# Kernel tuning notes

Hardware: AMD Instinct MI355X
Metric: run time of the kernel (lower is better)

Reference implementation:

```python
import jax, jax.numpy as jnp
import numpy as np

MASK_VALUE = -1e6


def setup_inputs() -> dict:
    key = jax.random.key(0)
    ks = jax.random.split(key, 8)
    B, Lq, Lk, D, H = 4, 512, 512, 128, 128
    return {
        "queries": jax.random.normal(ks[0], (B, Lq, D), dtype=jnp.float32),
        "keys": jax.random.normal(ks[1], (B, Lk, D), dtype=jnp.float32),
        "values": jax.random.normal(ks[2], (B, Lk, D), dtype=jnp.float32),
        "valid_seq_len": jax.random.randint(ks[3], (B,), 1, Lk + 1),
        "Wq": jax.random.normal(ks[4], (D, H), dtype=jnp.float32) * 0.05,
        "Wk": jax.random.normal(ks[5], (D, H), dtype=jnp.float32) * 0.05,
        "wv": jax.random.normal(ks[6], (H,), dtype=jnp.float32) * 0.05,
        "Wo": jax.random.normal(ks[7], (D, H), dtype=jnp.float32) * 0.05,
    }


def reference(queries, keys, values, valid_seq_len, Wq, Wk, wv, Wo):
    # q: (B,Lq,H), k: (B,Lk,H)
    q = jnp.einsum("bqd,dh->bqh", queries, Wq)
    k = jnp.einsum("bkd,dh->bkh", keys, Wk)
    # additive features: (B,Lq,Lk,H) -> scalar scores via wv
    feat = jnp.tanh(q[:, :, None, :] + k[:, None, :, :])
    scores = jnp.einsum("bqkh,h->bqk", feat, wv)
    # mask invalid key positions per batch (softmax over last dim)
    Lk = keys.shape[1]
    mask = jnp.arange(Lk)[None, None, :] < valid_seq_len[:, None, None]
    scores = jnp.where(mask, scores, MASK_VALUE)
    attn = jax.nn.softmax(scores, axis=-1)  # (B,Lq,Lk)
    out = jnp.einsum("bqk,bkd->bqd", attn, values)
    return jnp.einsum("bqd,dh->bqh", out, Wo)
```

## Files before the change

### kernel.cpp

```cpp
#include <hip/hip_runtime.h>
#include <hip/hip_bf16.h>

#define B_   4
#define LQ   512
#define LK   512
#define D_   128
#define H_   128
#define LKP  576
#define QSS  2
#define QSF  4

#define TWO_LOG2E 2.885390081777927f
#define LOG2E     1.442695040888963f

__device__ __forceinline__ float fexp2(float x) {
#if __has_builtin(__builtin_amdgcn_exp2f)
  return __builtin_amdgcn_exp2f(x);
#else
  return exp2f(x);
#endif
}
__device__ __forceinline__ float frcp(float x) {
#if __has_builtin(__builtin_amdgcn_rcpf)
  return __builtin_amdgcn_rcpf(x);
#else
  return __fdividef(1.0f, x);
#endif
}

__device__ __forceinline__ void sig4(float eqa, float eqb, float w, float2 ek,
                                     float& aA0, float& aA1, float& aB0, float& aB1) {
  float dA0 = fmaf(eqa, ek.x, 1.f);
  float dA1 = fmaf(eqa, ek.y, 1.f);
  float RA  = frcp(dA0 * dA1);
  aA0 = fmaf(w * dA1, RA, aA0);
  aA1 = fmaf(w * dA0, RA, aA1);
  float dB0 = fmaf(eqb, ek.x, 1.f);
  float dB1 = fmaf(eqb, ek.y, 1.f);
  float RB  = frcp(dB0 * dB1);
  aB0 = fmaf(w * dB1, RB, aB0);
  aB1 = fmaf(w * dB0, RB, aB1);
}

__global__ __launch_bounds__(256) void proj_kernel(
    const float* __restrict__ queries, const float* __restrict__ keys,
    const float* __restrict__ Wq, const float* __restrict__ Wk,
    float* __restrict__ Eq, float* __restrict__ EkT) {
  __shared__ float s_x[8][D_];
  int r0 = blockIdx.x * 8;
  bool qside = r0 < B_ * LQ;
  const float* X = qside ? queries : keys;
  const float* W = qside ? Wq : Wk;
  int rb = qside ? r0 : r0 - B_ * LQ;
  int tid = threadIdx.x;
  for (int i = tid; i < 8 * D_; i += 256)
    s_x[i >> 7][i & 127] = X[(size_t)(rb + (i >> 7)) * D_ + (i & 127)];
  __syncthreads();
  int h = tid & 127, rh = tid >> 7;
  const float4* x0 = (const float4*)s_x[rh * 4 + 0];
  const float4* x1 = (const float4*)s_x[rh * 4 + 1];
  const float4* x2 = (const float4*)s_x[rh * 4 + 2];
  const float4* x3 = (const float4*)s_x[rh * 4 + 3];
  float a0 = 0.f, a1 = 0.f, a2 = 0.f, a3 = 0.f;
  #pragma unroll 8
  for (int d4 = 0; d4 < D_ / 4; ++d4) {
    float4 xa = x0[d4], xb = x1[d4], xc = x2[d4], xd = x3[d4];
    const float* Wd = W + 4 * d4 * H_ + h;
    float w0 = Wd[0], w1 = Wd[H_], w2 = Wd[2 * H_], w3 = Wd[3 * H_];
    a0 = fmaf(xa.x, w0, fmaf(xa.y, w1, fmaf(xa.z, w2, fmaf(xa.w, w3, a0))));
    a1 = fmaf(xb.x, w0, fmaf(xb.y, w1, fmaf(xb.z, w2, fmaf(xb.w, w3, a1))));
    a2 = fmaf(xc.x, w0, fmaf(xc.y, w1, fmaf(xc.z, w2, fmaf(xc.w, w3, a2))));
    a3 = fmaf(xd.x, w0, fmaf(xd.y, w1, fmaf(xd.z, w2, fmaf(xd.w, w3, a3))));
  }
  if (qside) {
    Eq[(size_t)(rb + rh * 4 + 0) * H_ + h] = fexp2(a0 * TWO_LOG2E);
    Eq[(size_t)(rb + rh * 4 + 1) * H_ + h] = fexp2(a1 * TWO_LOG2E);
    Eq[(size_t)(rb + rh * 4 + 2) * H_ + h] = fexp2(a2 * TWO_LOG2E);
    Eq[(size_t)(rb + rh * 4 + 3) * H_ + h] = fexp2(a3 * TWO_LOG2E);
  } else {
    int b = rb >> 9, kk = (rb & 511) + rh * 4;
    float* dst = EkT + ((size_t)b * H_ + h) * LKP + kk;
    dst[0] = fexp2(a0 * TWO_LOG2E);
    dst[1] = fexp2(a1 * TWO_LOG2E);
    dst[2] = fexp2(a2 * TWO_LOG2E);
    dst[3] = fexp2(a3 * TWO_LOG2E);
  }
}

__global__ __launch_bounds__(256) void score_kernel(
    const float* __restrict__ Eq, const float* __restrict__ EkT,
    const int* __restrict__ vlen_arr, const float* __restrict__ wv,
    float* __restrict__ sc_g) {
  int id = blockIdx.x;
  int b = id & 3, q0 = (id >> 2) * QSS;
  int tid = threadIdx.x;

  __shared__ float s_eq[QSS][H_];
  __shared__ float s_wv[H_];

  s_eq[tid >> 7][tid & 127] = Eq[(size_t)(b * LQ + q0 + (tid >> 7)) * H_ + (tid & 127)];
  if (tid < H_) s_wv[tid] = wv[tid];
  __syncthreads();
  int vlen = vlen_arr[b];

  const float4* wv4p = (const float4*)s_wv;
  float sum_wv = 0.f;
  #pragma unroll
  for (int j = 0; j < H_ / 4; ++j) {
    float4 t4 = wv4p[j];
    sum_wv += t4.x + t4.y + t4.z + t4.w;
  }

  int k0 = tid * 2;
  if (k0 < vlen) {
    const float2* ek2 = (const float2*)(EkT + (size_t)b * H_ * LKP);
    const float4* eqa4 = (const float4*)s_eq[0];
    const float4* eqb4 = (const float4*)s_eq[1];
    float aA0 = 0.f, aA1 = 0.f, aB0 = 0.f, aB1 = 0.f;
    #pragma unroll 2
    for (int h4 = 0; h4 < H_ / 4; ++h4) {
      float2 e0 = ek2[(size_t)(4 * h4 + 0) * (LKP / 2) + tid];
      float2 e1 = ek2[(size_t)(4 * h4 + 1) * (LKP / 2) + tid];
      float2 e2 = ek2[(size_t)(4 * h4 + 2) * (LKP / 2) + tid];
      float2 e3 = ek2[(size_t)(4 * h4 + 3) * (LKP / 2) + tid];
      float4 w4 = wv4p[h4];
      float4 qa = eqa4[h4];
      float4 qb = eqb4[h4];
      sig4(qa.x, qb.x, w4.x, e0, aA0, aA1, aB0, aB1);
      sig4(qa.y, qb.y, w4.y, e1, aA0, aA1, aB0, aB1);
      sig4(qa.z, qb.z, w4.z, e2, aA0, aA1, aB0, aB1);
      sig4(qa.w, qb.w, w4.w, e3, aA0, aA1, aB0, aB1);
    }
    float2 rA = { fmaf(-2.f, aA0, sum_wv), fmaf(-2.f, aA1, sum_wv) };
    float2 rB = { fmaf(-2.f, aB0, sum_wv), fmaf(-2.f, aB1, sum_wv) };
    ((float2*)(sc_g + (size_t)(b * LQ + q0 + 0) * LK))[tid] = rA;
    ((float2*)(sc_g + (size_t)(b * LQ + q0 + 1) * LK))[tid] = rB;
  }
}

__global__ __launch_bounds__(256) void finish_kernel(
    const float* __restrict__ sc_g, const float* __restrict__ values,
    const int* __restrict__ vlen_arr, const float* __restrict__ Wo,
    float* __restrict__ out) {
  int id = blockIdx.x;
  int b = id & 3, q0 = (id >> 2) * QSF;
  int tid = threadIdx.x, wave = tid >> 6, lane = tid & 63;
  int vlen = vlen_arr[b];

  __shared__ float s_w[QSF][LK];
  __shared__ float s_po[QSF][QSF][D_];
  __shared__ float s_pr[QSF][D_];

  {
    const float* srow = sc_g + (size_t)(b * LQ + q0 + wave) * LK;
    float vals[LK / 64];
    float m = -3.0e38f;
    #pragma unroll
    for (int j = 0; j < LK / 64; ++j) {
      int k = lane + j * 64;
      float v = (k < vlen) ? srow[k] : -1.0e30f;
      vals[j] = v;
      m = fmaxf(m, v);
    }
    #pragma unroll
    for (int off = 32; off; off >>= 1) m = fmaxf(m, __shfl_xor(m, off));
    float sum = 0.f;
    #pragma unroll
    for (int j = 0; j < LK / 64; ++j) {
      float e = fexp2((vals[j] - m) * LOG2E);
      vals[j] = e;
      sum += e;
    }
    #pragma unroll
    for (int off = 32; off; off >>= 1) sum += __shfl_xor(sum, off);
    float inv = frcp(sum);
    #pragma unroll
    for (int j = 0; j < LK / 64; ++j) s_w[wave][lane + j * 64] = vals[j] * inv;
  }
  __syncthreads();

  {
    int kbeg = wave * 128;
    int kend = min((vlen + 3) & ~3, kbeg + 128);
    const float2* vrow = (const float2*)(values + (size_t)b * LK * D_);
    float2 a0 = {0.f, 0.f}, a1 = {0.f, 0.f}, a2 = {0.f, 0.f}, a3 = {0.f, 0.f};
    #pragma unroll 2
    for (int kk = kbeg; kk < kend; kk += 4) {
      float2 v0 = vrow[(size_t)(kk + 0) * 64 + lane];
      float2 v1 = vrow[(size_t)(kk + 1) * 64 + lane];
      float2 v2 = vrow[(size_t)(kk + 2) * 64 + lane];
      float2 v3 = vrow[(size_t)(kk + 3) * 64 + lane];
      float4 w0 = *(const float4*)&s_w[0][kk];
      float4 w1 = *(const float4*)&s_w[1][kk];
      float4 w2 = *(const float4*)&s_w[2][kk];
      float4 w3 = *(const float4*)&s_w[3][kk];
      a0.x += w0.x * v0.x + w0.y * v1.x + w0.z * v2.x + w0.w * v3.x;
      a0.y += w0.x * v0.y + w0.y * v1.y + w0.z * v2.y + w0.w * v3.y;
      a1.x += w1.x * v0.x + w1.y * v1.x + w1.z * v2.x + w1.w * v3.x;
      a1.y += w1.x * v0.y + w1.y * v1.y + w1.z * v2.y + w1.w * v3.y;
      a2.x += w2.x * v0.x + w2.y * v1.x + w2.z * v2.x + w2.w * v3.x;
      a2.y += w2.x * v0.y + w2.y * v1.y + w2.z * v2.y + w2.w * v3.y;
      a3.x += w3.x * v0.x + w3.y * v1.x + w3.z * v2.x + w3.w * v3.x;
      a3.y += w3.x * v0.y + w3.y * v1.y + w3.z * v2.y + w3.w * v3.y;
    }
    s_po[wave][0][2 * lane] = a0.x; s_po[wave][0][2 * lane + 1] = a0.y;
    s_po[wave][1][2 * lane] = a1.x; s_po[wave][1][2 * lane + 1] = a1.y;
    s_po[wave][2][2 * lane] = a2.x; s_po[wave][2][2 * lane + 1] = a2.y;
    s_po[wave][3][2 * lane] = a3.x; s_po[wave][3][2 * lane + 1] = a3.y;
  }
  __syncthreads();

  #pragma unroll
  for (int i = tid; i < QSF * D_; i += 256) {
    int r = i >> 7, d = i & 127;
    s_pr[r][d] = s_po[0][r][d] + s_po[1][r][d] + s_po[2][r][d] + s_po[3][r][d];
  }
  __syncthreads();

  {
    int h = tid & 127, r = tid >> 7;
    float accA = 0.f, accB = 0.f;
    #pragma unroll 8
    for (int d = 0; d < D_; ++d) {
      float w = Wo[d * H_ + h];
      accA = fmaf(s_pr[r][d], w, accA);
      accB = fmaf(s_pr[r + 2][d], w, accB);
    }
    out[(size_t)(b * LQ + q0 + r) * H_ + h] = accA;
    out[(size_t)(b * LQ + q0 + r + 2) * H_ + h] = accB;
  }
}

extern "C" void kernel_launch(void* const* d_in, const int* in_sizes, int n_in,
                              void* d_out, int out_size, void* d_ws, size_t ws_size,
                              hipStream_t stream) {
  const float* queries = (const float*)d_in[0];
  const float* keys    = (const float*)d_in[1];
  const float* values  = (const float*)d_in[2];
  const int*   vlen    = (const int*)d_in[3];
  const float* Wq      = (const float*)d_in[4];
  const float* Wk      = (const float*)d_in[5];
  const float* wv      = (const float*)d_in[6];
  const float* Wo      = (const float*)d_in[7];
  float* out = (float*)d_out;

  float* Eq   = (float*)d_ws;
  float* EkT  = Eq + (size_t)B_ * LQ * H_;
  float* sc_g = EkT + (size_t)B_ * H_ * LKP;

  proj_kernel<<<dim3(B_ * (LQ + LK) / 8), 256, 0, stream>>>(queries, keys, Wq, Wk, Eq, EkT);
  score_kernel<<<dim3(B_ * (LQ / QSS)), 256, 0, stream>>>(Eq, EkT, vlen, wv, sc_g);
  finish_kernel<<<dim3(B_ * (LQ / QSF)), 256, 0, stream>>>(sc_g, values, vlen, Wo, out);
}
```

Measured before the change: 117.2 us.

## Widen score and PV register tiles to float4 per thread

The score kernel now handles four query rows per block and four keys per thread, with float4 loads of EkT. Each loaded key vector is reused across two query rows per thread, and the number of score blocks is halved. The finish kernel's PV loop switches to float4 value loads, splitting the keys across half-waves, and combines the halves with a cross-lane shuffle. The aim is fewer load instructions and more register reuse, at the cost of higher register pressure and fewer blocks in the score grid.

```diff
diff --git a/kernel.cpp b/kernel.cpp
--- a/kernel.cpp
+++ b/kernel.cpp
@@ -7,7 +7,7 @@
 #define D_   128
 #define H_   128
 #define LKP  576
-#define QSS  2
+#define QSS  4
 #define QSF  4
 
 #define TWO_LOG2E 2.885390081777927f
@@ -28,18 +28,17 @@
 #endif
 }
 
-__device__ __forceinline__ void sig4(float eqa, float eqb, float w, float2 ek,
-                                     float& aA0, float& aA1, float& aB0, float& aB1) {
-  float dA0 = fmaf(eqa, ek.x, 1.f);
-  float dA1 = fmaf(eqa, ek.y, 1.f);
-  float RA  = frcp(dA0 * dA1);
-  aA0 = fmaf(w * dA1, RA, aA0);
-  aA1 = fmaf(w * dA0, RA, aA1);
-  float dB0 = fmaf(eqb, ek.x, 1.f);
-  float dB1 = fmaf(eqb, ek.y, 1.f);
-  float RB  = frcp(dB0 * dB1);
-  aB0 = fmaf(w * dB1, RB, aB0);
-  aB1 = fmaf(w * dB0, RB, aB1);
+__device__ __forceinline__ void sig4k(float eq, float w, float4 ek, float4& acc) {
+  float d0 = fmaf(eq, ek.x, 1.f);
+  float d1 = fmaf(eq, ek.y, 1.f);
+  float d2 = fmaf(eq, ek.z, 1.f);
+  float d3 = fmaf(eq, ek.w, 1.f);
+  float R01 = frcp(d0 * d1);
+  float R23 = frcp(d2 * d3);
+  acc.x = fmaf(w * d1, R01, acc.x);
+  acc.y = fmaf(w * d0, R01, acc.y);
+  acc.z = fmaf(w * d3, R23, acc.z);
+  acc.w = fmaf(w * d2, R23, acc.w);
 }
 
 __global__ __launch_bounds__(256) void proj_kernel(
@@ -98,7 +97,8 @@
   __shared__ float s_eq[QSS][H_];
   __shared__ float s_wv[H_];
 
-  s_eq[tid >> 7][tid & 127] = Eq[(size_t)(b * LQ + q0 + (tid >> 7)) * H_ + (tid & 127)];
+  for (int i = tid; i < QSS * H_; i += 256)
+    s_eq[i >> 7][i & 127] = Eq[(size_t)(b * LQ + q0 + (i >> 7)) * H_ + (i & 127)];
   if (tid < H_) s_wv[tid] = wv[tid];
   __syncthreads();
   int vlen = vlen_arr[b];
@@ -111,30 +111,34 @@
     sum_wv += t4.x + t4.y + t4.z + t4.w;
   }
 
-  int k0 = tid * 2;
+  int kq = tid & 127, rp = tid >> 7;
+  int k0 = kq * 4;
   if (k0 < vlen) {
-    const float2* ek2 = (const float2*)(EkT + (size_t)b * H_ * LKP);
-    const float4* eqa4 = (const float4*)s_eq[0];
-    const float4* eqb4 = (const float4*)s_eq[1];
-    float aA0 = 0.f, aA1 = 0.f, aB0 = 0.f, aB1 = 0.f;
+    const float4* ekp = (const float4*)(EkT + (size_t)b * H_ * LKP);
+    const float4* qa4 = (const float4*)s_eq[2 * rp + 0];
+    const float4* qb4 = (const float4*)s_eq[2 * rp + 1];
+    float4 accA = {0.f, 0.f, 0.f, 0.f};
+    float4 accB = {0.f, 0.f, 0.f, 0.f};
     #pragma unroll 2
     for (int h4 = 0; h4 < H_ / 4; ++h4) {
-      float2 e0 = ek2[(size_t)(4 * h4 + 0) * (LKP / 2) + tid];
-      float2 e1 = ek2[(size_t)(4 * h4 + 1) * (LKP / 2) + tid];
-      float2 e2 = ek2[(size_t)(4 * h4 + 2) * (LKP / 2) + tid];
-      float2 e3 = ek2[(size_t)(4 * h4 + 3) * (LKP / 2) + tid];
+      float4 e0 = ekp[(size_t)(4 * h4 + 0) * (LKP / 4) + kq];
+      float4 e1 = ekp[(size_t)(4 * h4 + 1) * (LKP / 4) + kq];
+      float4 e2 = ekp[(size_t)(4 * h4 + 2) * (LKP / 4) + kq];
+      float4 e3 = ekp[(size_t)(4 * h4 + 3) * (LKP / 4) + kq];
       float4 w4 = wv4p[h4];
-      float4 qa = eqa4[h4];
-      float4 qb = eqb4[h4];
-      sig4(qa.x, qb.x, w4.x, e0, aA0, aA1, aB0, aB1);
-      sig4(qa.y, qb.y, w4.y, e1, aA0, aA1, aB0, aB1);
-      sig4(qa.z, qb.z, w4.z, e2, aA0, aA1, aB0, aB1);
-      sig4(qa.w, qb.w, w4.w, e3, aA0, aA1, aB0, aB1);
-    }
-    float2 rA = { fmaf(-2.f, aA0, sum_wv), fmaf(-2.f, aA1, sum_wv) };
-    float2 rB = { fmaf(-2.f, aB0, sum_wv), fmaf(-2.f, aB1, sum_wv) };
-    ((float2*)(sc_g + (size_t)(b * LQ + q0 + 0) * LK))[tid] = rA;
-    ((float2*)(sc_g + (size_t)(b * LQ + q0 + 1) * LK))[tid] = rB;
+      float4 qa = qa4[h4];
+      float4 qb = qb4[h4];
+      sig4k(qa.x, w4.x, e0, accA);  sig4k(qb.x, w4.x, e0, accB);
+      sig4k(qa.y, w4.y, e1, accA);  sig4k(qb.y, w4.y, e1, accB);
+      sig4k(qa.z, w4.z, e2, accA);  sig4k(qb.z, w4.z, e2, accB);
+      sig4k(qa.w, w4.w, e3, accA);  sig4k(qb.w, w4.w, e3, accB);
+    }
+    float4 rA = { fmaf(-2.f, accA.x, sum_wv), fmaf(-2.f, accA.y, sum_wv),
+                  fmaf(-2.f, accA.z, sum_wv), fmaf(-2.f, accA.w, sum_wv) };
+    float4 rB = { fmaf(-2.f, accB.x, sum_wv), fmaf(-2.f, accB.y, sum_wv),
+                  fmaf(-2.f, accB.z, sum_wv), fmaf(-2.f, accB.w, sum_wv) };
+    ((float4*)(sc_g + (size_t)(b * LQ + q0 + 2 * rp + 0) * LK))[kq] = rA;
+    ((float4*)(sc_g + (size_t)(b * LQ + q0 + 2 * rp + 1) * LK))[kq] = rB;
   }
 }
 
@@ -182,31 +186,51 @@
   {
     int kbeg = wave * 128;
     int kend = min((vlen + 3) & ~3, kbeg + 128);
-    const float2* vrow = (const float2*)(values + (size_t)b * LK * D_);
-    float2 a0 = {0.f, 0.f}, a1 = {0.f, 0.f}, a2 = {0.f, 0.f}, a3 = {0.f, 0.f};
-    #pragma unroll 2
+    const float4* v4 = (const float4*)(values + (size_t)b * LK * D_);
+    int dq = lane & 31, kpar = lane >> 5;
+    float4 a0 = {0,0,0,0}, a1 = {0,0,0,0}, a2 = {0,0,0,0}, a3 = {0,0,0,0};
     for (int kk = kbeg; kk < kend; kk += 4) {
-      float2 v0 = vrow[(size_t)(kk + 0) * 64 + lane];
-      float2 v1 = vrow[(size_t)(kk + 1) * 64 + lane];
-      float2 v2 = vrow[(size_t)(kk + 2) * 64 + lane];
-      float2 v3 = vrow[(size_t)(kk + 3) * 64 + lane];
+      float4 va = v4[(size_t)(kk + 0 + kpar) * 32 + dq];
+      float4 vb = v4[(size_t)(kk + 2 + kpar) * 32 + dq];
       float4 w0 = *(const float4*)&s_w[0][kk];
       float4 w1 = *(const float4*)&s_w[1][kk];
       float4 w2 = *(const float4*)&s_w[2][kk];
       float4 w3 = *(const float4*)&s_w[3][kk];
-      a0.x += w0.x * v0.x + w0.y * v1.x + w0.z * v2.x + w0.w * v3.x;
-      a0.y += w0.x * v0.y + w0.y * v1.y + w0.z * v2.y + w0.w * v3.y;
-      a1.x += w1.x * v0.x + w1.y * v1.x + w1.z * v2.x + w1.w * v3.x;
-      a1.y += w1.x * v0.y + w1.y * v1.y + w1.z * v2.y + w1.w * v3.y;
-      a2.x += w2.x * v0.x + w2.y * v1.x + w2.z * v2.x + w2.w * v3.x;
-      a2.y += w2.x * v0.y + w2.y * v1.y + w2.z * v2.y + w2.w * v3.y;
-      a3.x += w3.x * v0.x + w3.y * v1.x + w3.z * v2.x + w3.w * v3.x;
-      a3.y += w3.x * v0.y + w3.y * v1.y + w3.z * v2.y + w3.w * v3.y;
-    }
-    s_po[wave][0][2 * lane] = a0.x; s_po[wave][0][2 * lane + 1] = a0.y;
-    s_po[wave][1][2 * lane] = a1.x; s_po[wave][1][2 * lane + 1] = a1.y;
-    s_po[wave][2][2 * lane] = a2.x; s_po[wave][2][2 * lane + 1] = a2.y;
-    s_po[wave][3][2 * lane] = a3.x; s_po[wave][3][2 * lane + 1] = a3.y;
+      float wa0 = kpar ? w0.y : w0.x, wb0 = kpar ? w0.w : w0.z;
+      float wa1 = kpar ? w1.y : w1.x, wb1 = kpar ? w1.w : w1.z;
+      float wa2 = kpar ? w2.y : w2.x, wb2 = kpar ? w2.w : w2.z;
+      float wa3 = kpar ? w3.y : w3.x, wb3 = kpar ? w3.w : w3.z;
+      a0.x = fmaf(wa0, va.x, fmaf(wb0, vb.x, a0.x));
+      a0.y = fmaf(wa0, va.y, fmaf(wb0, vb.y, a0.y));
+      a0.z = fmaf(wa0, va.z, fmaf(wb0, vb.z, a0.z));
+      a0.w = fmaf(wa0, va.w, fmaf(wb0, vb.w, a0.w));
+      a1.x = fmaf(wa1, va.x, fmaf(wb1, vb.x, a1.x));
+      a1.y = fmaf(wa1, va.y, fmaf(wb1, vb.y, a1.y));
+      a1.z = fmaf(wa1, va.z, fmaf(wb1, vb.z, a1.z));
+      a1.w = fmaf(wa1, va.w, fmaf(wb1, vb.w, a1.w));
+      a2.x = fmaf(wa2, va.x, fmaf(wb2, vb.x, a2.x));
+      a2.y = fmaf(wa2, va.y, fmaf(wb2, vb.y, a2.y));
+      a2.z = fmaf(wa2, va.z, fmaf(wb2, vb.z, a2.z));
+      a2.w = fmaf(wa2, va.w, fmaf(wb2, vb.w, a2.w));
+      a3.x = fmaf(wa3, va.x, fmaf(wb3, vb.x, a3.x));
+      a3.y = fmaf(wa3, va.y, fmaf(wb3, vb.y, a3.y));
+      a3.z = fmaf(wa3, va.z, fmaf(wb3, vb.z, a3.z));
+      a3.w = fmaf(wa3, va.w, fmaf(wb3, vb.w, a3.w));
+    }
+    a0.x += __shfl_xor(a0.x, 32); a0.y += __shfl_xor(a0.y, 32);
+    a0.z += __shfl_xor(a0.z, 32); a0.w += __shfl_xor(a0.w, 32);
+    a1.x += __shfl_xor(a1.x, 32); a1.y += __shfl_xor(a1.y, 32);
+    a1.z += __shfl_xor(a1.z, 32); a1.w += __shfl_xor(a1.w, 32);
+    a2.x += __shfl_xor(a2.x, 32); a2.y += __shfl_xor(a2.y, 32);
+    a2.z += __shfl_xor(a2.z, 32); a2.w += __shfl_xor(a2.w, 32);
+    a3.x += __shfl_xor(a3.x, 32); a3.y += __shfl_xor(a3.y, 32);
+    a3.z += __shfl_xor(a3.z, 32); a3.w += __shfl_xor(a3.w, 32);
+    if (lane < 32) {
+      ((float4*)s_po[wave][0])[dq] = a0;
+      ((float4*)s_po[wave][1])[dq] = a1;
+      ((float4*)s_po[wave][2])[dq] = a2;
+      ((float4*)s_po[wave][3])[dq] = a3;
+    }
   }
   __syncthreads();
 
```

After: 126.0 us. +7.5%, slower.
